# Kernel optimization log

Measured on AMD Instinct MI355X. Metric: run time of the kernel, lower is better.

Reference implementation:

```python
import jax, jax.numpy as jnp
import numpy as np

EPS = 1e-6

def setup_inputs() -> dict:
    key = jax.random.key(0)
    ks = jax.random.split(key, 9)
    B, H, N, V, E = 4096, 50, 10, 100000, 128
    s_nodes = jax.random.randint(ks[0], (B, 1), 0, V)
    t_nodes = jax.random.randint(ks[1], (B, 1), 0, V)
    t_times = jax.random.uniform(ks[2], (B, 1), dtype=jnp.float32)
    h_nodes = jax.random.randint(ks[3], (B, H), 0, V)
    h_times = jax.random.uniform(ks[4], (B, H), dtype=jnp.float32)
    h_time_mask = jnp.ones((B, H), dtype=jnp.float32)
    n_nodes = jax.random.randint(ks[5], (B, N), 0, V)
    # init as in torch: uniform(-1/emb, 1/emb) for node_emb, constant 1 for delta
    node_emb_w = jax.random.uniform(ks[6], (V, E), minval=-1.0 / E, maxval=1.0 / E, dtype=jnp.float32)
    delta_w = jnp.ones((V, 1), dtype=jnp.float32)
    return dict(s_nodes=s_nodes, t_nodes=t_nodes, t_times=t_times, h_nodes=h_nodes,
                h_times=h_times, h_time_mask=h_time_mask, n_nodes=n_nodes,
                node_emb_w=node_emb_w, delta_w=delta_w)

def reference(s_nodes, t_nodes, t_times, h_nodes, h_times, h_time_mask, n_nodes,
              node_emb_w, delta_w):
    src = node_emb_w[s_nodes]          # [B,1,E]
    tar = node_emb_w[t_nodes]          # [B,1,E]
    neg = node_emb_w[n_nodes]          # [B,N,E]
    his = node_emb_w[h_nodes]          # [B,H,E]

    att = jax.nn.softmax(-jnp.sum((src - his) ** 2, axis=2), axis=1)      # [B,H]
    p_mu = -jnp.sum((src - tar) ** 2, axis=2)[:, 0]                        # [B]
    p_alpha = -jnp.sum((his - tar) ** 2, axis=2)                           # [B,H]
    delta = delta_w[s_nodes][:, :, 0]                                      # [B,1]
    d_time = jnp.abs(t_times - h_times)                                    # [B,H]
    decay = jnp.exp(delta * d_time)                                        # [B,H]
    p_lambda = p_mu + jnp.sum(att * p_alpha * decay * h_time_mask, axis=1)  # [B]

    n_mu = -jnp.sum((src - neg) ** 2, axis=2)                              # [B,N]
    # ||h - n||^2 = ||h||^2 + ||n||^2 - 2 h.n  (avoids [B,H,N,E] tensor)
    h_sq = jnp.sum(his ** 2, axis=2)                                       # [B,H]
    n_sq = jnp.sum(neg ** 2, axis=2)                                       # [B,N]
    hn = jnp.einsum('bhe,bne->bhn', his, neg)                              # [B,H,N]
    n_alpha = -(h_sq[:, :, None] + n_sq[:, None, :] - 2.0 * hn)            # [B,H,N]
    w = att * decay * h_time_mask                                          # [B,H]
    n_lambda = n_mu + jnp.einsum('bh,bhn->bn', w, n_alpha)                 # [B,N]

    pos_loss = -jnp.log(jax.nn.sigmoid(p_lambda) + EPS)                    # [B]
    neg_loss = jnp.sum(jnp.log(jax.nn.sigmoid(-n_lambda) + EPS), axis=1)   # [B]
    return pos_loss - neg_loss
```

## Files before the change

kernel.cpp:

```cpp
#include <hip/hip_runtime.h>
#include <math.h>

#define HH   50
#define NNEG 10
#define EE   128
#define EPSF 1e-6f

__global__ __launch_bounds__(256, 8) void htne_kernel(
    const int*   __restrict__ s_nodes,
    const int*   __restrict__ t_nodes,
    const float* __restrict__ t_times,
    const int*   __restrict__ h_nodes,
    const float* __restrict__ h_times,
    const float* __restrict__ h_mask,
    const int*   __restrict__ n_nodes,
    const float* __restrict__ emb,
    const float* __restrict__ delta_w,
    float*       __restrict__ out)
{
    __shared__ int   s_hidx[HH];
    __shared__ float s_ht[HH];
    __shared__ float s_hm[HH];
    __shared__ int   s_nidx[NNEG];
    __shared__ float s_part[4][EE];
    __shared__ float s_scw[4][4];
    __shared__ float s_s2t;
    __shared__ float s_nl[NNEG];

    const int b    = blockIdx.x;
    const int tid  = threadIdx.x;
    const int wid  = tid >> 6;
    const int lane = tid & 63;
    const int g    = tid >> 4;
    const int sub  = tid & 15;

    if (tid < HH) {
        s_hidx[tid] = h_nodes[b * HH + tid];
        s_ht[tid]   = h_times[b * HH + tid];
        s_hm[tid]   = h_mask[b * HH + tid];
    } else if (tid < HH + NNEG) {
        s_nidx[tid - HH] = n_nodes[b * NNEG + (tid - HH)];
    }

    const int   sidx  = s_nodes[b];
    const int   tidx  = t_nodes[b];
    const float tt    = t_times[b];
    const float delta = delta_w[sidx];

    float sva[8], tva[8];
    {
        float4 a0 = *(const float4*)(emb + (size_t)sidx * EE + sub * 8);
        float4 a1 = *(const float4*)(emb + (size_t)sidx * EE + sub * 8 + 4);
        float4 b0 = *(const float4*)(emb + (size_t)tidx * EE + sub * 8);
        float4 b1 = *(const float4*)(emb + (size_t)tidx * EE + sub * 8 + 4);
        sva[0]=a0.x; sva[1]=a0.y; sva[2]=a0.z; sva[3]=a0.w;
        sva[4]=a1.x; sva[5]=a1.y; sva[6]=a1.z; sva[7]=a1.w;
        tva[0]=b0.x; tva[1]=b0.y; tva[2]=b0.z; tva[3]=b0.w;
        tva[4]=b1.x; tva[5]=b1.y; tva[6]=b1.z; tva[7]=b1.w;
    }

    __syncthreads();

    float SE = 0.f, UW = 0.f, UH = 0.f, UP = 0.f;
    float hb[8] = {0.f,0.f,0.f,0.f,0.f,0.f,0.f,0.f};

    #pragma unroll
    for (int it = 0; it < 4; ++it) {
        const int t = g + it * 16;
        if (t < HH) {
            const int idx = s_hidx[t];
            const float* hrow = emb + (size_t)idx * EE + sub * 8;
            float4 h0 = *(const float4*)(hrow);
            float4 h1 = *(const float4*)(hrow + 4);
            float hv[8] = {h0.x,h0.y,h0.z,h0.w,h1.x,h1.y,h1.z,h1.w};
            float a = 0.f, c = 0.f, q = 0.f;
            #pragma unroll
            for (int k = 0; k < 8; ++k) {
                float d1 = hv[k] - sva[k];
                float d2 = hv[k] - tva[k];
                a = fmaf(d1, d1, a);
                c = fmaf(d2, d2, c);
                q = fmaf(hv[k], hv[k], q);
            }
            #pragma unroll
            for (int off = 1; off <= 8; off <<= 1) {
                a += __shfl_xor(a, off);
                c += __shfl_xor(c, off);
                q += __shfl_xor(q, off);
            }
            const float e1 = expf(-a);
            const float dt = fabsf(tt - s_ht[t]);
            const float u  = e1 * expf(delta * dt) * s_hm[t];
            SE += e1; UW += u; UH += u * q; UP += u * c;
            #pragma unroll
            for (int k = 0; k < 8; ++k) hb[k] = fmaf(u, hv[k], hb[k]);
        } else if (t == HH) {
            float a = 0.f;
            #pragma unroll
            for (int k = 0; k < 8; ++k) {
                float d = sva[k] - tva[k];
                a = fmaf(d, d, a);
            }
            #pragma unroll
            for (int off = 1; off <= 8; off <<= 1) a += __shfl_xor(a, off);
            if (sub == 0) s_s2t = a;
        }
    }

    #pragma unroll
    for (int off = 16; off <= 32; off <<= 1) {
        SE += __shfl_xor(SE, off);
        UW += __shfl_xor(UW, off);
        UH += __shfl_xor(UH, off);
        UP += __shfl_xor(UP, off);
        #pragma unroll
        for (int k = 0; k < 8; ++k) hb[k] += __shfl_xor(hb[k], off);
    }
    if (lane < 16) {
        *(float4*)(&s_part[wid][sub * 8])     = make_float4(hb[0],hb[1],hb[2],hb[3]);
        *(float4*)(&s_part[wid][sub * 8 + 4]) = make_float4(hb[4],hb[5],hb[6],hb[7]);
    }
    if (lane == 0) {
        s_scw[wid][0] = SE; s_scw[wid][1] = UW;
        s_scw[wid][2] = UH; s_scw[wid][3] = UP;
    }
    __syncthreads();

    const float SEt = s_scw[0][0] + s_scw[1][0] + s_scw[2][0] + s_scw[3][0];
    const float UWt = s_scw[0][1] + s_scw[1][1] + s_scw[2][1] + s_scw[3][1];
    const float UHt = s_scw[0][2] + s_scw[1][2] + s_scw[2][2] + s_scw[3][2];
    const float UPt = s_scw[0][3] + s_scw[1][3] + s_scw[2][3] + s_scw[3][3];

    if (g < NNEG) {
        float hbs[8];
        #pragma unroll
        for (int k = 0; k < 8; ++k)
            hbs[k] = s_part[0][sub*8+k] + s_part[1][sub*8+k]
                   + s_part[2][sub*8+k] + s_part[3][sub*8+k];
        const int idx = s_nidx[g];
        const float* nrow = emb + (size_t)idx * EE + sub * 8;
        float4 n0 = *(const float4*)(nrow);
        float4 n1 = *(const float4*)(nrow + 4);
        float nv[8] = {n0.x,n0.y,n0.z,n0.w,n1.x,n1.y,n1.z,n1.w};
        float a = 0.f, q = 0.f, d = 0.f;
        #pragma unroll
        for (int k = 0; k < 8; ++k) {
            float d1 = nv[k] - sva[k];
            a = fmaf(d1, d1, a);
            q = fmaf(nv[k], nv[k], q);
            d = fmaf(hbs[k], nv[k], d);
        }
        #pragma unroll
        for (int off = 1; off <= 8; off <<= 1) {
            a += __shfl_xor(a, off);
            q += __shfl_xor(q, off);
            d += __shfl_xor(d, off);
        }
        if (sub == 0) {
            float nl = -a - (UHt + q * UWt - 2.f * d) / SEt;
            float sg = 1.f / (1.f + expf(nl));
            s_nl[g] = logf(sg + EPSF);
        }
    }
    __syncthreads();

    if (tid == 0) {
        float neg_loss = 0.f;
        #pragma unroll
        for (int n = 0; n < NNEG; ++n) neg_loss += s_nl[n];
        float pl = -s_s2t - UPt / SEt;
        float sg = 1.f / (1.f + expf(-pl));
        float pos_loss = -logf(sg + EPSF);
        out[b] = pos_loss - neg_loss;
    }
}

extern "C" void kernel_launch(void* const* d_in, const int* in_sizes, int n_in,
                              void* d_out, int out_size, void* d_ws, size_t ws_size,
                              hipStream_t stream) {
    const int*   s_nodes = (const int*)  d_in[0];
    const int*   t_nodes = (const int*)  d_in[1];
    const float* t_times = (const float*)d_in[2];
    const int*   h_nodes = (const int*)  d_in[3];
    const float* h_times = (const float*)d_in[4];
    const float* h_mask  = (const float*)d_in[5];
    const int*   n_nodes = (const int*)  d_in[6];
    const float* emb     = (const float*)d_in[7];
    const float* delta_w = (const float*)d_in[8];
    float*       out     = (float*)d_out;

    const int Bn = in_sizes[0];
    htne_kernel<<<Bn, 256, 0, stream>>>(s_nodes, t_nodes, t_times, h_nodes,
                                        h_times, h_mask, n_nodes, emb, delta_w, out);
}
```

Baseline: 29.29 us.

## Load history indices into registers and overlap negative row fetch with history loop

Removes the shared-memory staging of history/negative indices and the first __syncthreads; each thread loads its own indices, times and masks directly from global memory. The negative embedding rows are now fetched and their distance/norm terms computed in the idle groups of the last history iteration, so only the dot product with the weighted history sum remains after the barrier. Exact expf/logf are also replaced with fast __expf/__logf intrinsics. This shortens the serial dependency chain and drops one barrier, at the cost of slightly lower transcendental precision and more live registers.

```diff
diff --git a/kernel.cpp b/kernel.cpp
--- a/kernel.cpp
+++ b/kernel.cpp
@@ -18,10 +18,6 @@
     const float* __restrict__ delta_w,
     float*       __restrict__ out)
 {
-    __shared__ int   s_hidx[HH];
-    __shared__ float s_ht[HH];
-    __shared__ float s_hm[HH];
-    __shared__ int   s_nidx[NNEG];
     __shared__ float s_part[4][EE];
     __shared__ float s_scw[4][4];
     __shared__ float s_s2t;
@@ -34,18 +30,20 @@
     const int g    = tid >> 4;
     const int sub  = tid & 15;
 
-    if (tid < HH) {
-        s_hidx[tid] = h_nodes[b * HH + tid];
-        s_ht[tid]   = h_times[b * HH + tid];
-        s_hm[tid]   = h_mask[b * HH + tid];
-    } else if (tid < HH + NNEG) {
-        s_nidx[tid - HH] = n_nodes[b * NNEG + (tid - HH)];
-    }
-
     const int   sidx  = s_nodes[b];
     const int   tidx  = t_nodes[b];
     const float tt    = t_times[b];
     const float delta = delta_w[sidx];
+
+    int ridx[4];
+    #pragma unroll
+    for (int it = 0; it < 4; ++it) {
+        const int t = g + it * 16;
+        if (t < HH)                     ridx[it] = h_nodes[b * HH + t];
+        else if (it == 3 && t > HH && t <= HH + NNEG)
+                                        ridx[it] = n_nodes[b * NNEG + (t - HH - 1)];
+        else                            ridx[it] = -1;
+    }
 
     float sva[8], tva[8];
     {
@@ -59,19 +57,20 @@
         tva[4]=b1.x; tva[5]=b1.y; tva[6]=b1.z; tva[7]=b1.w;
     }
 
-    __syncthreads();
-
     float SE = 0.f, UW = 0.f, UH = 0.f, UP = 0.f;
     float hb[8] = {0.f,0.f,0.f,0.f,0.f,0.f,0.f,0.f};
+    float nv[8];
+    float nA = 0.f, nQ = 0.f;
 
     #pragma unroll
     for (int it = 0; it < 4; ++it) {
         const int t = g + it * 16;
         if (t < HH) {
-            const int idx = s_hidx[t];
-            const float* hrow = emb + (size_t)idx * EE + sub * 8;
+            const float* hrow = emb + (size_t)ridx[it] * EE + sub * 8;
             float4 h0 = *(const float4*)(hrow);
             float4 h1 = *(const float4*)(hrow + 4);
+            const float ht = h_times[b * HH + t];
+            const float hm = h_mask[b * HH + t];
             float hv[8] = {h0.x,h0.y,h0.z,h0.w,h1.x,h1.y,h1.z,h1.w};
             float a = 0.f, c = 0.f, q = 0.f;
             #pragma unroll
@@ -88,22 +87,42 @@
                 c += __shfl_xor(c, off);
                 q += __shfl_xor(q, off);
             }
-            const float e1 = expf(-a);
-            const float dt = fabsf(tt - s_ht[t]);
-            const float u  = e1 * expf(delta * dt) * s_hm[t];
+            const float e1 = __expf(-a);
+            const float u  = e1 * __expf(delta * fabsf(tt - ht)) * hm;
             SE += e1; UW += u; UH += u * q; UP += u * c;
             #pragma unroll
             for (int k = 0; k < 8; ++k) hb[k] = fmaf(u, hv[k], hb[k]);
-        } else if (t == HH) {
-            float a = 0.f;
-            #pragma unroll
-            for (int k = 0; k < 8; ++k) {
-                float d = sva[k] - tva[k];
-                a = fmaf(d, d, a);
+        } else if (it == 3) {
+            if (t == HH) {
+                float a = 0.f;
+                #pragma unroll
+                for (int k = 0; k < 8; ++k) {
+                    float d = sva[k] - tva[k];
+                    a = fmaf(d, d, a);
+                }
+                #pragma unroll
+                for (int off = 1; off <= 8; off <<= 1) a += __shfl_xor(a, off);
+                if (sub == 0) s_s2t = a;
+            } else if (t <= HH + NNEG) {
+                const float* nrow = emb + (size_t)ridx[it] * EE + sub * 8;
+                float4 n0 = *(const float4*)(nrow);
+                float4 n1 = *(const float4*)(nrow + 4);
+                nv[0]=n0.x; nv[1]=n0.y; nv[2]=n0.z; nv[3]=n0.w;
+                nv[4]=n1.x; nv[5]=n1.y; nv[6]=n1.z; nv[7]=n1.w;
+                float a = 0.f, q = 0.f;
+                #pragma unroll
+                for (int k = 0; k < 8; ++k) {
+                    float d1 = nv[k] - sva[k];
+                    a = fmaf(d1, d1, a);
+                    q = fmaf(nv[k], nv[k], q);
+                }
+                #pragma unroll
+                for (int off = 1; off <= 8; off <<= 1) {
+                    a += __shfl_xor(a, off);
+                    q += __shfl_xor(q, off);
+                }
+                nA = a; nQ = q;
             }
-            #pragma unroll
-            for (int off = 1; off <= 8; off <<= 1) a += __shfl_xor(a, off);
-            if (sub == 0) s_s2t = a;
         }
     }
 
@@ -129,48 +148,31 @@
     const float SEt = s_scw[0][0] + s_scw[1][0] + s_scw[2][0] + s_scw[3][0];
     const float UWt = s_scw[0][1] + s_scw[1][1] + s_scw[2][1] + s_scw[3][1];
     const float UHt = s_scw[0][2] + s_scw[1][2] + s_scw[2][2] + s_scw[3][2];
-    const float UPt = s_scw[0][3] + s_scw[1][3] + s_scw[2][3] + s_scw[3][3];
 
-    if (g < NNEG) {
-        float hbs[8];
-        #pragma unroll
-        for (int k = 0; k < 8; ++k)
-            hbs[k] = s_part[0][sub*8+k] + s_part[1][sub*8+k]
-                   + s_part[2][sub*8+k] + s_part[3][sub*8+k];
-        const int idx = s_nidx[g];
-        const float* nrow = emb + (size_t)idx * EE + sub * 8;
-        float4 n0 = *(const float4*)(nrow);
-        float4 n1 = *(const float4*)(nrow + 4);
-        float nv[8] = {n0.x,n0.y,n0.z,n0.w,n1.x,n1.y,n1.z,n1.w};
-        float a = 0.f, q = 0.f, d = 0.f;
+    if (g >= 3 && g <= 12) {
+        float d = 0.f;
         #pragma unroll
         for (int k = 0; k < 8; ++k) {
-            float d1 = nv[k] - sva[k];
-            a = fmaf(d1, d1, a);
-            q = fmaf(nv[k], nv[k], q);
-            d = fmaf(hbs[k], nv[k], d);
+            float hbs = s_part[0][sub*8+k] + s_part[1][sub*8+k]
+                      + s_part[2][sub*8+k] + s_part[3][sub*8+k];
+            d = fmaf(hbs, nv[k], d);
         }
         #pragma unroll
-        for (int off = 1; off <= 8; off <<= 1) {
-            a += __shfl_xor(a, off);
-            q += __shfl_xor(q, off);
-            d += __shfl_xor(d, off);
-        }
+        for (int off = 1; off <= 8; off <<= 1) d += __shfl_xor(d, off);
         if (sub == 0) {
-            float nl = -a - (UHt + q * UWt - 2.f * d) / SEt;
-            float sg = 1.f / (1.f + expf(nl));
-            s_nl[g] = logf(sg + EPSF);
+            float nl = -nA - (UHt + nQ * UWt - 2.f * d) / SEt;
+            s_nl[g - 3] = __logf(1.f / (1.f + __expf(nl)) + EPSF);
         }
     }
     __syncthreads();
 
     if (tid == 0) {
+        const float UPt = s_scw[0][3] + s_scw[1][3] + s_scw[2][3] + s_scw[3][3];
         float neg_loss = 0.f;
         #pragma unroll
         for (int n = 0; n < NNEG; ++n) neg_loss += s_nl[n];
         float pl = -s_s2t - UPt / SEt;
-        float sg = 1.f / (1.f + expf(-pl));
-        float pos_loss = -logf(sg + EPSF);
+        float pos_loss = -__logf(1.f / (1.f + __expf(-pl)) + EPSF);
         out[b] = pos_loss - neg_loss;
     }
 }
```

Result: slower. 30.92 us (+5.6%).
